# Optimization experiments

Hardware: AMD Instinct MI355X
Metric: run time of the kernel (lower is better)

The kernel has to match this reference:

```python
import jax, jax.numpy as jnp
import numpy as np

N_NODES = 50000
N_EDGES = 1600000
IN_CH = 128
HIDDEN = 64
OUT_DIM = 64
N_GRAPHS = 64


def setup_inputs() -> dict:
    key = jax.random.key(0)
    ks = jax.random.split(key, 8)
    x = jax.random.normal(ks[0], (N_NODES, IN_CH), dtype=jnp.float32)
    W1 = jax.random.normal(ks[1], (IN_CH, HIDDEN), dtype=jnp.float32) * (1.0 / np.sqrt(IN_CH))
    b1 = jnp.zeros((HIDDEN,), dtype=jnp.float32)
    W2 = jax.random.normal(ks[2], (HIDDEN, HIDDEN), dtype=jnp.float32) * (1.0 / np.sqrt(HIDDEN))
    b2 = jnp.zeros((HIDDEN,), dtype=jnp.float32)
    Wp = jax.random.normal(ks[3], (HIDDEN, OUT_DIM), dtype=jnp.float32) * (1.0 / np.sqrt(HIDDEN))
    bp = jnp.zeros((OUT_DIM,), dtype=jnp.float32)
    edge_index = jax.random.randint(ks[4], (2, N_EDGES), 0, N_NODES, dtype=jnp.int32)
    batch = jnp.sort(jax.random.randint(ks[5], (N_NODES,), 0, N_GRAPHS, dtype=jnp.int32))
    return {"x": x, "W1": W1, "b1": b1, "W2": W2, "b2": b2,
            "Wp": Wp, "bp": bp, "edge_index": edge_index, "batch": batch}


def _gcn_norm(edge_index, num_nodes):
    # add self-loops, then symmetric normalization D^{-1/2} (A+I) D^{-1/2}
    loop = jnp.arange(num_nodes, dtype=edge_index.dtype)
    src = jnp.concatenate([edge_index[0], loop])
    dst = jnp.concatenate([edge_index[1], loop])
    deg = jax.ops.segment_sum(jnp.ones_like(dst, dtype=jnp.float32), dst,
                              num_segments=num_nodes)
    dinv = jnp.where(deg > 0, jax.lax.rsqrt(deg), 0.0)
    norm = dinv[src] * dinv[dst]  # [E+N]
    return src, dst, norm


def _gcn_conv(x, W, b, src, dst, norm, num_nodes):
    h = x @ W                                  # [N, F_out] transform first (F_out small)
    msg = h[src] * norm[:, None]               # gather + scale  [E+N, F_out]
    agg = jax.ops.segment_sum(msg, dst, num_segments=num_nodes)
    return agg + b


def reference(x, W1, b1, W2, b2, Wp, bp, edge_index, batch):
    n = x.shape[0]
    src, dst, norm = _gcn_norm(edge_index, n)
    h = jax.nn.relu(_gcn_conv(x, W1, b1, src, dst, norm, n))
    # dropout: eval mode (identity)
    h = jax.nn.relu(_gcn_conv(h, W2, b2, src, dst, norm, n))
    # global mean pool over graphs in batch
    gsum = jax.ops.segment_sum(h, batch, num_segments=N_GRAPHS)
    cnt = jax.ops.segment_sum(jnp.ones((n,), dtype=h.dtype), batch,
                              num_segments=N_GRAPHS)
    g = gsum / jnp.maximum(cnt, 1.0)[:, None]
    return g @ Wp + bp
```

## Files before the change

### kernel.cpp

```cpp
#include <hip/hip_runtime.h>

#define N_NODES  50000
#define N_EDGESC 1600000
#define N_GRAPHS 64
#define NBUCK    196
#define BCAP     10240
#define CHUNK    2048

static __device__ __forceinline__ unsigned short f2bf(float f) {
  unsigned u = __float_as_uint(f);
  u += 0x7FFF + ((u >> 16) & 1);
  return (unsigned short)(u >> 16);
}
static __device__ __forceinline__ float bfLo(unsigned u) {
  return __uint_as_float(u << 16);
}
static __device__ __forceinline__ float bfHi(unsigned u) {
  return __uint_as_float(u & 0xFFFF0000u);
}

static __device__ __forceinline__ int lowerb(const int* a, int n, int v) {
  int lo = 0, hi = n;
  while (lo < hi) { int m = (lo + hi) >> 1; if (a[m] < v) lo = m + 1; else hi = m; }
  return lo;
}

__global__ void k_zero(int* __restrict__ gcur, float* __restrict__ gsum) {
  int t = blockIdx.x * 256 + threadIdx.x;
  if (t < NBUCK) gcur[t] = 0;
  if (t < N_GRAPHS * 64) gsum[t] = 0.f;
}

__global__ __launch_bounds__(256) void k_bucket(const int* __restrict__ src,
                                                const int* __restrict__ dst,
                                                int* __restrict__ gcur,
                                                unsigned* __restrict__ bbuf, int E) {
  __shared__ int hist[NBUCK], base[NBUCK], cur[NBUCK];
  int t = threadIdx.x;
  if (t < NBUCK) { hist[t] = 0; cur[t] = 0; }
  __syncthreads();
  int e0 = blockIdx.x * CHUNK;
#pragma unroll
  for (int i = 0; i < CHUNK; i += 256) {
    int e = e0 + i + t;
    if (e < E) atomicAdd(&hist[dst[e] >> 8], 1);
  }
  __syncthreads();
  if (t < NBUCK) base[t] = hist[t] ? atomicAdd(&gcur[t], hist[t]) : 0;
  __syncthreads();
#pragma unroll
  for (int i = 0; i < CHUNK; i += 256) {
    int e = e0 + i + t;
    if (e < E) {
      int d = dst[e], b = d >> 8;
      int pos = base[b] + atomicAdd(&cur[b], 1);
      unsigned packed = ((unsigned)(d & 255) << 24) | (unsigned)src[e];
      if (pos < BCAP) bbuf[(size_t)b * BCAP + pos] = packed;
    }
  }
}

__global__ void k_bscan(const int* __restrict__ gcur, int* __restrict__ boff) {
  __shared__ int sm[256];
  int t = threadIdx.x;
  int v = (t < NBUCK) ? gcur[t] : 0;
  sm[t] = v;
  __syncthreads();
  for (int o = 1; o < 256; o <<= 1) {
    int add = (t >= o) ? sm[t - o] : 0;
    __syncthreads();
    sm[t] += add;
    __syncthreads();
  }
  if (t < NBUCK) boff[t] = sm[t] - v;
}

__global__ __launch_bounds__(256) void k_bsort(const unsigned* __restrict__ bbuf,
                                               const int* __restrict__ gcur,
                                               const int* __restrict__ boff,
                                               int* __restrict__ csr,
                                               int* __restrict__ row_off,
                                               float* __restrict__ dinv, int E) {
  __shared__ int hist[256], off[256], cur[256];
  int b = blockIdx.x, t = threadIdx.x;
  hist[t] = 0; cur[t] = 0;
  __syncthreads();
  int cnt = min(gcur[b], BCAP);
  const unsigned* bp = bbuf + (size_t)b * BCAP;
  for (int i = t; i < cnt; i += 256) atomicAdd(&hist[bp[i] >> 24], 1);
  __syncthreads();
  off[t] = hist[t];
  __syncthreads();
  for (int o = 1; o < 256; o <<= 1) {
    int add = (t >= o) ? off[t - o] : 0;
    __syncthreads();
    off[t] += add;
    __syncthreads();
  }
  int excl = off[t] - hist[t];
  __syncthreads();
  off[t] = excl;
  __syncthreads();
  int gb = boff[b];
  int idx = (b << 8) + t;
  if (idx <= N_NODES) row_off[idx] = gb + off[t];
  if (idx < N_NODES)  dinv[idx] = rsqrtf((float)(hist[t] + 1));
  for (int i = t; i < cnt; i += 256) {
    unsigned v = bp[i];
    int ld = v >> 24;
    int pos = atomicAdd(&cur[ld], 1);
    csr[gb + off[ld] + pos] = (int)(v & 0xFFFFFFu);
  }
}

template <int K>
__global__ __launch_bounds__(256) void k_gemm(const float* __restrict__ x,
                                              const float* __restrict__ W,
                                              const float* __restrict__ dinv,
                                              unsigned short* __restrict__ out, int N) {
  constexpr int KS = 64;
  constexpr int KP = KS + 4;
  __shared__ float xs[64 * KP];
  __shared__ float Wl[KS * 64];
  const int t = threadIdx.x;
  const int lane = t & 63;
  const int w = t >> 6;
  const int n0 = blockIdx.x * 64;

  float acc[16];
#pragma unroll
  for (int j = 0; j < 16; ++j) acc[j] = 0.f;

  for (int h = 0; h < K / KS; ++h) {
#pragma unroll
    for (int i = 0; i < KS * 16 / 256; ++i) {
      int li = i * 256 + t;
      float4 v = reinterpret_cast<const float4*>(W + h * KS * 64)[li];
      *reinterpret_cast<float4*>(Wl + li * 4) = v;
    }
#pragma unroll
    for (int i = 0; i < 64 * (KS / 4) / 256; ++i) {
      int li = i * 256 + t;
      int row = li / (KS / 4), c4 = li % (KS / 4);
      int node = n0 + row;
      float4 v = make_float4(0.f, 0.f, 0.f, 0.f);
      if (node < N) v = reinterpret_cast<const float4*>(x + (size_t)node * K + h * KS)[c4];
      *reinterpret_cast<float4*>(xs + row * KP + c4 * 4) = v;
    }
    __syncthreads();

    const float* xr = xs + lane * KP;
    const float* wq = Wl + w * 16;
#pragma unroll 4
    for (int kp = 0; kp < KS / 4; ++kp) {
      float4 xv = *reinterpret_cast<const float4*>(xr + kp * 4);
#pragma unroll
      for (int q = 0; q < 4; ++q) {
        int k = kp * 4 + q;
        float xq = (q == 0) ? xv.x : (q == 1) ? xv.y : (q == 2) ? xv.z : xv.w;
        const float* wk = wq + k * 64;
        float4 w0 = *reinterpret_cast<const float4*>(wk);
        float4 w1 = *reinterpret_cast<const float4*>(wk + 4);
        float4 w2 = *reinterpret_cast<const float4*>(wk + 8);
        float4 w3 = *reinterpret_cast<const float4*>(wk + 12);
        acc[ 0] = fmaf(xq, w0.x, acc[ 0]);
        acc[ 1] = fmaf(xq, w0.y, acc[ 1]);
        acc[ 2] = fmaf(xq, w0.z, acc[ 2]);
        acc[ 3] = fmaf(xq, w0.w, acc[ 3]);
        acc[ 4] = fmaf(xq, w1.x, acc[ 4]);
        acc[ 5] = fmaf(xq, w1.y, acc[ 5]);
        acc[ 6] = fmaf(xq, w1.z, acc[ 6]);
        acc[ 7] = fmaf(xq, w1.w, acc[ 7]);
        acc[ 8] = fmaf(xq, w2.x, acc[ 8]);
        acc[ 9] = fmaf(xq, w2.y, acc[ 9]);
        acc[10] = fmaf(xq, w2.z, acc[10]);
        acc[11] = fmaf(xq, w2.w, acc[11]);
        acc[12] = fmaf(xq, w3.x, acc[12]);
        acc[13] = fmaf(xq, w3.y, acc[13]);
        acc[14] = fmaf(xq, w3.z, acc[14]);
        acc[15] = fmaf(xq, w3.w, acc[15]);
      }
    }
    __syncthreads();
  }

  int node = n0 + lane;
  if (node < N) {
    float dv = dinv[node];
    unsigned pk[8];
#pragma unroll
    for (int j = 0; j < 8; ++j) {
      unsigned lo = f2bf(acc[2 * j] * dv);
      unsigned hi = f2bf(acc[2 * j + 1] * dv);
      pk[j] = lo | (hi << 16);
    }
    unsigned* op = reinterpret_cast<unsigned*>(out + (size_t)node * 64 + w * 16);
    *reinterpret_cast<uint4*>(op)     = make_uint4(pk[0], pk[1], pk[2], pk[3]);
    *reinterpret_cast<uint4*>(op + 4) = make_uint4(pk[4], pk[5], pk[6], pk[7]);
  }
}

__global__ __launch_bounds__(256) void k_gather(const unsigned short* __restrict__ hs,
                                                const int* __restrict__ row_off,
                                                const int* __restrict__ csr,
                                                const float* __restrict__ dinv,
                                                const float* __restrict__ bias,
                                                float* __restrict__ out, int N) {
  const int lane = threadIdx.x & 63;
  const int half = lane >> 5;
  const int cl   = lane & 31;
  int wid = blockIdx.x * 4 + (threadIdx.x >> 6);
  int stride = gridDim.x * 4;
  const unsigned* hsd = reinterpret_cast<const unsigned*>(hs);
  float b0 = bias[2 * cl], b1 = bias[2 * cl + 1];
  for (int i = wid; i < N; i += stride) {
    float acc0 = 0.f, acc1 = 0.f;
    {
      unsigned sd = hsd[(((unsigned)i) << 5) + cl];
      if (half == 0) { acc0 = bfLo(sd); acc1 = bfHi(sd); }
    }
    const int s0 = row_off[i], s1 = row_off[i + 1];
    int j = s0;
    for (; j + 32 <= s1; j += 32) {
      int idx[16];
#pragma unroll
      for (int q = 0; q < 16; ++q) idx[q] = csr[j + 2 * q + half];
      unsigned v[16];
#pragma unroll
      for (int q = 0; q < 16; ++q)
        v[q] = hsd[(((unsigned)idx[q]) << 5) + cl];
#pragma unroll
      for (int q = 0; q < 16; ++q) { acc0 += bfLo(v[q]); acc1 += bfHi(v[q]); }
    }
    if (j < s1) {
      int idx[16];
      bool ok[16];
#pragma unroll
      for (int q = 0; q < 16; ++q) {
        int e = j + 2 * q + half;
        ok[q] = e < s1;
        idx[q] = csr[min(e, s1 - 1)];
      }
      unsigned v[16];
#pragma unroll
      for (int q = 0; q < 16; ++q)
        v[q] = hsd[(((unsigned)idx[q]) << 5) + cl];
#pragma unroll
      for (int q = 0; q < 16; ++q) {
        if (ok[q]) { acc0 += bfLo(v[q]); acc1 += bfHi(v[q]); }
      }
    }
    acc0 += __shfl_xor(acc0, 32);
    acc1 += __shfl_xor(acc1, 32);
    if (half == 0) {
      float dv = dinv[i];
      float r0 = fmaxf(fmaf(acc0, dv, b0), 0.0f);
      float r1 = fmaxf(fmaf(acc1, dv, b1), 0.0f);
      *reinterpret_cast<float2*>(out + (((size_t)i) << 6) + 2 * cl) = make_float2(r0, r1);
    }
  }
}

__global__ __launch_bounds__(256) void k_pool1(const float* __restrict__ h,
                                               const int* __restrict__ batch,
                                               float* __restrict__ gsum, int N) {
  int c = threadIdx.x & 63;
  int w = threadIdx.x >> 6;
  int r0 = blockIdx.x * 64 + w * 16;
  if (r0 >= N) return;
  int r1 = min(r0 + 16, N);
  int gprev = batch[r0];
  float acc = 0.f;
  for (int r = r0; r < r1; ++r) {
    int g = batch[r];
    if (g != gprev) { atomicAdd(&gsum[gprev * 64 + c], acc); acc = 0.f; gprev = g; }
    acc += h[(size_t)r * 64 + c];
  }
  atomicAdd(&gsum[gprev * 64 + c], acc);
}

__global__ void k_cnt(const int* __restrict__ batch, float* __restrict__ cinv, int N) {
  int g = threadIdx.x;
  int lo = lowerb(batch, N, g);
  int hi = lowerb(batch, N, g + 1);
  cinv[g] = 1.0f / fmaxf((float)(hi - lo), 1.0f);
}

__global__ void k_final(const float* __restrict__ gsum, const float* __restrict__ cinv,
                        const float* __restrict__ Wp, const float* __restrict__ bp,
                        float* __restrict__ out) {
  int idx = blockIdx.x * 256 + threadIdx.x;
  int g = idx >> 6, o = idx & 63;
  float acc = 0.f;
#pragma unroll
  for (int k = 0; k < 64; ++k) acc += gsum[g * 64 + k] * Wp[k * 64 + o];
  out[idx] = fmaf(acc, cinv[g], bp[o]);
}

extern "C" void kernel_launch(void* const* d_in, const int* in_sizes, int n_in,
                              void* d_out, int out_size, void* d_ws, size_t ws_size,
                              hipStream_t stream) {
  const float* x    = (const float*)d_in[0];
  const float* W1   = (const float*)d_in[1];
  const float* b1   = (const float*)d_in[2];
  const float* W2   = (const float*)d_in[3];
  const float* b2   = (const float*)d_in[4];
  const float* Wp   = (const float*)d_in[5];
  const float* bp   = (const float*)d_in[6];
  const int*   ei   = (const int*)d_in[7];
  const int*   batch= (const int*)d_in[8];
  float* out = (float*)d_out;

  const int N = N_NODES, E = N_EDGESC;
  const int* src  = ei;
  const int* dstp = ei + E;

  char* wsb = (char*)d_ws;
  size_t o = 0;
  auto alloc = [&](size_t bytes) -> void* {
    void* p = wsb + o;
    o = (o + bytes + 255) & ~(size_t)255;
    return p;
  };
  int*      gcur   = (int*)alloc(NBUCK * 4);
  int*      boff   = (int*)alloc(NBUCK * 4);
  unsigned* bbuf   = (unsigned*)alloc((size_t)NBUCK * BCAP * 4);
  int*      row_off= (int*)alloc((size_t)(N + 1) * 4);
  int*      csr    = (int*)alloc((size_t)E * 4);
  float*    dinv   = (float*)alloc((size_t)N * 4);
  unsigned short* bufBF = (unsigned short*)alloc((size_t)N * 64 * 2);
  float*    bufF   = (float*)alloc((size_t)N * 64 * 4);
  float*    gsum   = (float*)alloc(64 * 64 * 4);
  float*    cinv   = (float*)alloc(64 * 4);

  int gA = (E + CHUNK - 1) / CHUNK;
  int gN64 = (N + 63) / 64;

  k_zero<<<(N_GRAPHS * 64 + 255) / 256, 256, 0, stream>>>(gcur, gsum);
  k_bucket<<<gA, 256, 0, stream>>>(src, dstp, gcur, bbuf, E);
  k_bscan<<<1, 256, 0, stream>>>(gcur, boff);
  k_bsort<<<NBUCK, 256, 0, stream>>>(bbuf, gcur, boff, csr, row_off, dinv, E);

  k_gemm<128><<<gN64, 256, 0, stream>>>(x, W1, dinv, bufBF, N);
  k_gather<<<2048, 256, 0, stream>>>(bufBF, row_off, csr, dinv, b1, bufF, N);
  k_gemm<64><<<gN64, 256, 0, stream>>>(bufF, W2, dinv, bufBF, N);
  k_gather<<<2048, 256, 0, stream>>>(bufBF, row_off, csr, dinv, b2, bufF, N);

  k_pool1<<<gN64, 256, 0, stream>>>(bufF, batch, gsum, N);
  k_cnt<<<1, 64, 0, stream>>>(batch, cinv, N);
  k_final<<<16, 256, 0, stream>>>(gsum, cinv, Wp, bp, out);
}
```

Before: 192.5 us.

## Replace atomic bucket partition with per-block histogram, scan, and deterministic scatter

```diff
diff --git a/kernel.cpp b/kernel.cpp
--- a/kernel.cpp
+++ b/kernel.cpp
@@ -4,8 +4,8 @@
 #define N_EDGESC 1600000
 #define N_GRAPHS 64
 #define NBUCK    196
-#define BCAP     10240
 #define CHUNK    2048
+#define NBLK     782
 
 static __device__ __forceinline__ unsigned short f2bf(float f) {
   unsigned u = __float_as_uint(f);
@@ -25,87 +25,128 @@
   return lo;
 }
 
-__global__ void k_zero(int* __restrict__ gcur, float* __restrict__ gsum) {
-  int t = blockIdx.x * 256 + threadIdx.x;
-  if (t < NBUCK) gcur[t] = 0;
-  if (t < N_GRAPHS * 64) gsum[t] = 0.f;
-}
-
-__global__ __launch_bounds__(256) void k_bucket(const int* __restrict__ src,
-                                                const int* __restrict__ dst,
-                                                int* __restrict__ gcur,
-                                                unsigned* __restrict__ bbuf, int E) {
-  __shared__ int hist[NBUCK], base[NBUCK], cur[NBUCK];
-  int t = threadIdx.x;
-  if (t < NBUCK) { hist[t] = 0; cur[t] = 0; }
-  __syncthreads();
-  int e0 = blockIdx.x * CHUNK;
+__global__ __launch_bounds__(256) void k_hist(const int* __restrict__ dst,
+                                              int* __restrict__ bcnt,
+                                              float* __restrict__ gsum, int E) {
+  __shared__ int hist[NBUCK];
+  int t = threadIdx.x, blk = blockIdx.x;
+  if (t < NBUCK) hist[t] = 0;
+  if (blk == 0) {
+    for (int i = t; i < N_GRAPHS * 64; i += 256) gsum[i] = 0.f;
+  }
+  __syncthreads();
+  int e0 = blk * CHUNK;
 #pragma unroll
   for (int i = 0; i < CHUNK; i += 256) {
     int e = e0 + i + t;
     if (e < E) atomicAdd(&hist[dst[e] >> 8], 1);
   }
   __syncthreads();
-  if (t < NBUCK) base[t] = hist[t] ? atomicAdd(&gcur[t], hist[t]) : 0;
-  __syncthreads();
+  if (t < NBUCK) bcnt[(size_t)t * NBLK + blk] = hist[t];
+}
+
+__global__ __launch_bounds__(256) void k_cscan(int* __restrict__ bcnt,
+                                               int* __restrict__ btot) {
+  __shared__ int sm[256];
+  int b = blockIdx.x, t = threadIdx.x;
+  int* p = bcnt + (size_t)b * NBLK;
+  int carry = 0;
+  for (int tile = 0; tile < (NBLK + 255) / 256; ++tile) {
+    int idx = tile * 256 + t;
+    int v = (idx < NBLK) ? p[idx] : 0;
+    sm[t] = v;
+    __syncthreads();
+    for (int o = 1; o < 256; o <<= 1) {
+      int add = (t >= o) ? sm[t - o] : 0;
+      __syncthreads();
+      sm[t] += add;
+      __syncthreads();
+    }
+    int incl = sm[t];
+    int total = sm[255];
+    if (idx < NBLK) p[idx] = incl - v + carry;
+    carry += total;
+    __syncthreads();
+  }
+  if (t == 0) btot[b] = carry;
+}
+
+__global__ __launch_bounds__(256) void k_scatter(const int* __restrict__ src,
+                                                 const int* __restrict__ dst,
+                                                 const int* __restrict__ bcnt,
+                                                 const int* __restrict__ btot,
+                                                 unsigned* __restrict__ bbuf, int E) {
+  __shared__ int base[NBUCK], cur[NBUCK], sm[256];
+  int t = threadIdx.x, blk = blockIdx.x;
+  int v = (t < NBUCK) ? btot[t] : 0;
+  sm[t] = v;
+  __syncthreads();
+  for (int o = 1; o < 256; o <<= 1) {
+    int add = (t >= o) ? sm[t - o] : 0;
+    __syncthreads();
+    sm[t] += add;
+    __syncthreads();
+  }
+  if (t < NBUCK) {
+    base[t] = (sm[t] - v) + bcnt[(size_t)t * NBLK + blk];
+    cur[t] = 0;
+  }
+  __syncthreads();
+  int e0 = blk * CHUNK;
 #pragma unroll
   for (int i = 0; i < CHUNK; i += 256) {
     int e = e0 + i + t;
     if (e < E) {
       int d = dst[e], b = d >> 8;
       int pos = base[b] + atomicAdd(&cur[b], 1);
-      unsigned packed = ((unsigned)(d & 255) << 24) | (unsigned)src[e];
-      if (pos < BCAP) bbuf[(size_t)b * BCAP + pos] = packed;
-    }
-  }
-}
-
-__global__ void k_bscan(const int* __restrict__ gcur, int* __restrict__ boff) {
-  __shared__ int sm[256];
-  int t = threadIdx.x;
-  int v = (t < NBUCK) ? gcur[t] : 0;
-  sm[t] = v;
-  __syncthreads();
-  for (int o = 1; o < 256; o <<= 1) {
-    int add = (t >= o) ? sm[t - o] : 0;
-    __syncthreads();
-    sm[t] += add;
-    __syncthreads();
-  }
-  if (t < NBUCK) boff[t] = sm[t] - v;
-}
-
-__global__ __launch_bounds__(256) void k_bsort(const unsigned* __restrict__ bbuf,
-                                               const int* __restrict__ gcur,
-                                               const int* __restrict__ boff,
+      bbuf[pos] = ((unsigned)(d & 255) << 24) | (unsigned)src[e];
+    }
+  }
+}
+
+__global__ __launch_bounds__(512) void k_bsort(const unsigned* __restrict__ bbuf,
+                                               const int* __restrict__ btot,
                                                int* __restrict__ csr,
                                                int* __restrict__ row_off,
-                                               float* __restrict__ dinv, int E) {
-  __shared__ int hist[256], off[256], cur[256];
+                                               float* __restrict__ dinv) {
+  __shared__ int hist[256], off[256], cur[256], sm[256];
   int b = blockIdx.x, t = threadIdx.x;
-  hist[t] = 0; cur[t] = 0;
-  __syncthreads();
-  int cnt = min(gcur[b], BCAP);
-  const unsigned* bp = bbuf + (size_t)b * BCAP;
-  for (int i = t; i < cnt; i += 256) atomicAdd(&hist[bp[i] >> 24], 1);
-  __syncthreads();
-  off[t] = hist[t];
+  if (t < 256) {
+    int v = (t < NBUCK) ? btot[t] : 0;
+    sm[t] = v;
+    hist[t] = 0; cur[t] = 0;
+  }
   __syncthreads();
   for (int o = 1; o < 256; o <<= 1) {
-    int add = (t >= o) ? off[t - o] : 0;
-    __syncthreads();
-    off[t] += add;
-    __syncthreads();
-  }
-  int excl = off[t] - hist[t];
-  __syncthreads();
-  off[t] = excl;
-  __syncthreads();
-  int gb = boff[b];
-  int idx = (b << 8) + t;
-  if (idx <= N_NODES) row_off[idx] = gb + off[t];
-  if (idx < N_NODES)  dinv[idx] = rsqrtf((float)(hist[t] + 1));
-  for (int i = t; i < cnt; i += 256) {
+    int add = 0;
+    if (t < 256 && t >= o) add = sm[t - o];
+    __syncthreads();
+    if (t < 256) sm[t] += add;
+    __syncthreads();
+  }
+  int gb = (b > 0) ? sm[b - 1] : 0;
+  int cnt = btot[b];
+  const unsigned* bp = bbuf + gb;
+  for (int i = t; i < cnt; i += 512) atomicAdd(&hist[bp[i] >> 24], 1);
+  __syncthreads();
+  if (t < 256) off[t] = hist[t];
+  __syncthreads();
+  for (int o = 1; o < 256; o <<= 1) {
+    int add = 0;
+    if (t < 256 && t >= o) add = off[t - o];
+    __syncthreads();
+    if (t < 256) off[t] += add;
+    __syncthreads();
+  }
+  if (t < 256) {
+    int excl = off[t] - hist[t];
+    off[t] = excl;
+    int idx = (b << 8) + t;
+    if (idx <= N_NODES) row_off[idx] = gb + excl;
+    if (idx < N_NODES)  dinv[idx] = rsqrtf((float)(hist[t] + 1));
+  }
+  __syncthreads();
+  for (int i = t; i < cnt; i += 512) {
     unsigned v = bp[i];
     int ld = v >> 24;
     int pos = atomicAdd(&cur[ld], 1);
@@ -279,22 +320,21 @@
   atomicAdd(&gsum[gprev * 64 + c], acc);
 }
 
-__global__ void k_cnt(const int* __restrict__ batch, float* __restrict__ cinv, int N) {
-  int g = threadIdx.x;
-  int lo = lowerb(batch, N, g);
-  int hi = lowerb(batch, N, g + 1);
-  cinv[g] = 1.0f / fmaxf((float)(hi - lo), 1.0f);
-}
-
-__global__ void k_final(const float* __restrict__ gsum, const float* __restrict__ cinv,
+__global__ void k_final(const float* __restrict__ gsum, const int* __restrict__ batch,
                         const float* __restrict__ Wp, const float* __restrict__ bp,
-                        float* __restrict__ out) {
-  int idx = blockIdx.x * 256 + threadIdx.x;
-  int g = idx >> 6, o = idx & 63;
+                        float* __restrict__ out, int N) {
+  __shared__ int lb[5];
+  int t = threadIdx.x;
+  int g0 = blockIdx.x * 4;
+  if (t < 5) lb[t] = lowerb(batch, N, g0 + t);
+  __syncthreads();
+  int idx = blockIdx.x * 256 + t;
+  int g = idx >> 6, o = idx & 63, gl = g & 3;
+  float cinv = 1.0f / fmaxf((float)(lb[gl + 1] - lb[gl]), 1.0f);
   float acc = 0.f;
 #pragma unroll
   for (int k = 0; k < 64; ++k) acc += gsum[g * 64 + k] * Wp[k * 64 + o];
-  out[idx] = fmaf(acc, cinv[g], bp[o]);
+  out[idx] = fmaf(acc, cinv, bp[o]);
 }
 
 extern "C" void kernel_launch(void* const* d_in, const int* in_sizes, int n_in,
@@ -322,24 +362,22 @@
     o = (o + bytes + 255) & ~(size_t)255;
     return p;
   };
-  int*      gcur   = (int*)alloc(NBUCK * 4);
-  int*      boff   = (int*)alloc(NBUCK * 4);
-  unsigned* bbuf   = (unsigned*)alloc((size_t)NBUCK * BCAP * 4);
+  int*      bcnt   = (int*)alloc((size_t)NBUCK * NBLK * 4);
+  int*      btot   = (int*)alloc(NBUCK * 4);
+  unsigned* bbuf   = (unsigned*)alloc((size_t)E * 4);
   int*      row_off= (int*)alloc((size_t)(N + 1) * 4);
   int*      csr    = (int*)alloc((size_t)E * 4);
   float*    dinv   = (float*)alloc((size_t)N * 4);
   unsigned short* bufBF = (unsigned short*)alloc((size_t)N * 64 * 2);
   float*    bufF   = (float*)alloc((size_t)N * 64 * 4);
   float*    gsum   = (float*)alloc(64 * 64 * 4);
-  float*    cinv   = (float*)alloc(64 * 4);
-
-  int gA = (E + CHUNK - 1) / CHUNK;
+
   int gN64 = (N + 63) / 64;
 
-  k_zero<<<(N_GRAPHS * 64 + 255) / 256, 256, 0, stream>>>(gcur, gsum);
-  k_bucket<<<gA, 256, 0, stream>>>(src, dstp, gcur, bbuf, E);
-  k_bscan<<<1, 256, 0, stream>>>(gcur, boff);
-  k_bsort<<<NBUCK, 256, 0, stream>>>(bbuf, gcur, boff, csr, row_off, dinv, E);
+  k_hist<<<NBLK, 256, 0, stream>>>(dstp, bcnt, gsum, E);
+  k_cscan<<<NBUCK, 256, 0, stream>>>(bcnt, btot);
+  k_scatter<<<NBLK, 256, 0, stream>>>(src, dstp, bcnt, btot, bbuf, E);
+  k_bsort<<<NBUCK, 512, 0, stream>>>(bbuf, btot, csr, row_off, dinv);
 
   k_gemm<128><<<gN64, 256, 0, stream>>>(x, W1, dinv, bufBF, N);
   k_gather<<<2048, 256, 0, stream>>>(bufBF, row_off, csr, dinv, b1, bufF, N);
@@ -347,6 +385,5 @@
   k_gather<<<2048, 256, 0, stream>>>(bufBF, row_off, csr, dinv, b2, bufF, N);
 
   k_pool1<<<gN64, 256, 0, stream>>>(bufF, batch, gsum, N);
-  k_cnt<<<1, 64, 0, stream>>>(batch, cinv, N);
-  k_final<<<16, 256, 0, stream>>>(gsum, cinv, Wp, bp, out);
-}
+  k_final<<<16, 256, 0, stream>>>(gsum, batch, Wp, bp, out, N);
+}
```

Measured after the change: 173.1 us. 10.1% less time.
